# Kernel tuning notes

Measured on AMD Instinct MI355X. Metric: run time of the kernel, lower is better.

## Reference

```python
import jax, jax.numpy as jnp
import numpy as np

EPS = 1e-5


def setup_inputs() -> dict:
    key = jax.random.key(0)
    k1, k2 = jax.random.split(key)
    M, K, N = 8192, 4096, 11008  # tokens, in_features, out_features
    x = jax.random.normal(k1, (M, K), dtype=jnp.float32)
    w = jax.random.normal(k2, (N, K), dtype=jnp.float32)  # Linear weight [out, in]
    return {"x": x, "w": w}


def reference(x, w):
    # --- weight quantization (done once in __init__ in the torch module) ---
    # per-output-channel abs-max scale, clamped
    w_scales = jnp.maximum(jnp.max(jnp.abs(w), axis=1, keepdims=True), EPS) / 127.0  # [N,1]
    w_int8 = jnp.round(w / w_scales).astype(jnp.int8)  # [N,K]

    # --- dynamic per-token activation quantization ---
    x_scales = jnp.maximum(jnp.max(jnp.abs(x), axis=-1, keepdims=True), EPS) / 127.0  # [M,1]
    x_int8 = jnp.round(x / x_scales).astype(jnp.int8)  # [M,K]

    # --- int8 GEMM with int32 accumulation (torch._int_mm) ---
    out_int32 = jnp.matmul(x_int8.astype(jnp.int32), w_int8.T.astype(jnp.int32))  # [M,N]

    # --- dequantize: per-token scale x per-channel scale ---
    return out_int32.astype(x.dtype) * (x_scales * w_scales.reshape(1, -1))
```

## Files before the change

kernel.cpp:

```cpp
#include <hip/hip_runtime.h>
#include <hip/hip_bf16.h>


#define QEPS 1e-5f

using int4v = __attribute__((ext_vector_type(4))) int;

typedef __attribute__((address_space(3))) signed char lds_i8_t;
typedef __attribute__((address_space(1))) const signed char glb_i8_t;

__global__ __launch_bounds__(256) void quant_rows_k(const float* __restrict__ in,
                                                    signed char* __restrict__ out8,
                                                    float* __restrict__ scales) {
    const int K = 4096;
    const int row = blockIdx.x;
    const int t = threadIdx.x;
    const float4* in4 = (const float4*)(in + (size_t)row * K);
    float4 v[4];
    float amax = 0.f;
#pragma unroll
    for (int j = 0; j < 4; ++j) {
        v[j] = in4[t + 256 * j];
        amax = fmaxf(amax, fmaxf(fmaxf(fabsf(v[j].x), fabsf(v[j].y)),
                                 fmaxf(fabsf(v[j].z), fabsf(v[j].w))));
    }
#pragma unroll
    for (int off = 32; off > 0; off >>= 1)
        amax = fmaxf(amax, __shfl_xor(amax, off));
    __shared__ float wmax[4];
    if ((t & 63) == 0) wmax[t >> 6] = amax;
    __syncthreads();
    amax = fmaxf(fmaxf(wmax[0], wmax[1]), fmaxf(wmax[2], wmax[3]));
    const float scale = fmaxf(amax, QEPS) / 127.0f;
    if (t == 0) scales[row] = scale;
    char4* o4 = (char4*)(out8 + (size_t)row * K);
#pragma unroll
    for (int j = 0; j < 4; ++j) {
        char4 q;
        q.x = (signed char)(int)rintf(v[j].x / scale);
        q.y = (signed char)(int)rintf(v[j].y / scale);
        q.z = (signed char)(int)rintf(v[j].z / scale);
        q.w = (signed char)(int)rintf(v[j].w / scale);
        o4[t + 256 * j] = q;
    }
}

__global__ __launch_bounds__(512, 2) void gemm_i8_256(const signed char* __restrict__ A,
                                                      const signed char* __restrict__ B,
                                                      const float* __restrict__ xs,
                                                      const float* __restrict__ wsc,
                                                      float* __restrict__ C) {
    constexpr int K = 4096;
    constexpr int N = 11008;
    constexpr int BK = 128;
    constexpr int NT = K / BK;
    constexpr int TILE = 256 * 128;

    __shared__ __align__(16) signed char lds[4 * TILE];
    signed char* const la0 = lds;
    signed char* const la1 = lds + TILE;
    signed char* const lb0 = lds + 2 * TILE;
    signed char* const lb1 = lds + 3 * TILE;

    const int t = threadIdx.x;
    const int lane = t & 63;
    const int wid = t >> 6;
    const int wr = wid >> 2;
    const int wc = wid & 3;

    const int wg = (blockIdx.x & 7) * ((int)gridDim.x >> 3) + ((int)blockIdx.x >> 3);
    const int by = wg / 43;
    const int bx = wg - by * 43;
    const int brow = by * 256;
    const int bcol = bx * 256;

    const int srow = t >> 3;
    const int scol = ((t & 7) * 16) ^ ((srow & 7) << 4);
    const signed char* aptr = A + (size_t)(brow + srow) * K + scol;
    const signed char* bptr = B + (size_t)(bcol + srow) * K + scol;

    const int arow0 = wr * 128 + (lane & 15);
    const int bcol0 = wc * 64 + (lane & 15);
    const int kgrp = (lane >> 4) * 16;
    const int sw = (lane & 7) << 4;

    int4v acc[8][4];
#pragma unroll
    for (int m = 0; m < 8; ++m)
#pragma unroll
        for (int n = 0; n < 4; ++n) acc[m][n] = (int4v){0, 0, 0, 0};

#define STAGE(LA, LB, KT)                                                                  \
    do {                                                                                   \
        _Pragma("unroll") for (int j = 0; j < 4; ++j)                                      \
            __builtin_amdgcn_global_load_lds(                                              \
                (glb_i8_t*)(aptr + (size_t)(j * 64) * K + (size_t)(KT)*BK),                \
                (lds_i8_t*)((LA) + (j * 512 + t) * 16), 16, 0, 0);                         \
        _Pragma("unroll") for (int j = 0; j < 4; ++j)                                      \
            __builtin_amdgcn_global_load_lds(                                              \
                (glb_i8_t*)(bptr + (size_t)(j * 64) * K + (size_t)(KT)*BK),                \
                (lds_i8_t*)((LB) + (j * 512 + t) * 16), 16, 0, 0);                         \
    } while (0)

    auto compute_tile = [&](const signed char* LA, const signed char* LB) {
#pragma unroll
        for (int ks = 0; ks < 2; ++ks) {
            int4v bf[4];
#pragma unroll
            for (int n = 0; n < 4; ++n)
                bf[n] = *(const int4v*)(LB + (bcol0 + n * 16) * 128 + ((ks * 64 + kgrp) ^ sw));
#pragma unroll
            for (int mh = 0; mh < 2; ++mh) {
                int4v af[4];
#pragma unroll
                for (int mi = 0; mi < 4; ++mi)
                    af[mi] = *(const int4v*)(LA + (arow0 + (mh * 4 + mi) * 16) * 128 +
                                             ((ks * 64 + kgrp) ^ sw));
                __builtin_amdgcn_s_setprio(1);
#pragma unroll
                for (int mi = 0; mi < 4; ++mi)
#pragma unroll
                    for (int n = 0; n < 4; ++n)
                        acc[mh * 4 + mi][n] = __builtin_amdgcn_mfma_i32_16x16x64_i8(
                            af[mi], bf[n], acc[mh * 4 + mi][n], 0, 0, 0);
                __builtin_amdgcn_s_setprio(0);
            }
        }
    };

    STAGE(la0, lb0, 0);
    STAGE(la1, lb1, 1);
    asm volatile("s_waitcnt vmcnt(8)" ::: "memory");
    __builtin_amdgcn_s_barrier();

#pragma unroll 1
    for (int kt = 0; kt < NT; kt += 2) {
        compute_tile(la0, lb0);
        __builtin_amdgcn_s_barrier();
        STAGE(la0, lb0, (kt + 2) & (NT - 1));
        asm volatile("s_waitcnt vmcnt(8)" ::: "memory");
        __builtin_amdgcn_s_barrier();
        compute_tile(la1, lb1);
        __builtin_amdgcn_s_barrier();
        STAGE(la1, lb1, (kt + 3) & (NT - 1));
        asm volatile("s_waitcnt vmcnt(8)" ::: "memory");
        __builtin_amdgcn_s_barrier();
    }
#undef STAGE

    const int rgrp = (lane >> 4) * 4;
    float wsv[4];
#pragma unroll
    for (int n = 0; n < 4; ++n) wsv[n] = wsc[bcol + wc * 64 + n * 16 + (lane & 15)];
#pragma unroll
    for (int m = 0; m < 8; ++m) {
#pragma unroll
        for (int r = 0; r < 4; ++r) {
            const int row = brow + wr * 128 + m * 16 + rgrp + r;
            const float xsv = xs[row];
            const size_t base = (size_t)row * N + bcol + wc * 64 + (lane & 15);
#pragma unroll
            for (int n = 0; n < 4; ++n)
                C[base + n * 16] = (float)acc[m][n][r] * (xsv * wsv[n]);
        }
    }
}

extern "C" void kernel_launch(void* const* d_in, const int* in_sizes, int n_in,
                              void* d_out, int out_size, void* d_ws, size_t ws_size,
                              hipStream_t stream) {
    const float* x = (const float*)d_in[0];
    const float* w = (const float*)d_in[1];
    float* out = (float*)d_out;

    const int K = 4096;
    const int M = in_sizes[0] / K;
    const int N = in_sizes[1] / K;

    signed char* x8 = (signed char*)d_ws;
    signed char* w8 = x8 + (size_t)M * K;
    float* xscales = (float*)(w8 + (size_t)N * K);
    float* wscales = xscales + M;

    quant_rows_k<<<M, 256, 0, stream>>>(x, x8, xscales);
    quant_rows_k<<<N, 256, 0, stream>>>(w, w8, wscales);
    const int nwg = (M / 256) * (N / 256);
    gemm_i8_256<<<nwg, 512, 0, stream>>>(x8, w8, xscales, wscales, out);
}
```

Measured before the change: 480.5 us.

## Interleave global-to-LDS prefetch with MFMA in four phases per K-tile

Restructures the int8 GEMM main loop into four phases per 128-wide K tile. Each phase loads fragments from LDS, issues part of the next tile's global_load_lds, then runs 16 MFMAs, so memory traffic is spread across compute instead of issued in bulk between tiles. The LDS layout changes to two 64-byte K halves per buffer without XOR swizzling, which may bring back LDS bank conflicts on fragment reads. It also adds more barriers per tile.

```diff
diff --git a/kernel.cpp b/kernel.cpp
--- a/kernel.cpp
+++ b/kernel.cpp
@@ -45,22 +45,18 @@
     }
 }
 
-__global__ __launch_bounds__(512, 2) void gemm_i8_256(const signed char* __restrict__ A,
+__global__ __launch_bounds__(512, 2) void gemm_i8_8ph(const signed char* __restrict__ A,
                                                       const signed char* __restrict__ B,
                                                       const float* __restrict__ xs,
                                                       const float* __restrict__ wsc,
                                                       float* __restrict__ C) {
     constexpr int K = 4096;
     constexpr int N = 11008;
-    constexpr int BK = 128;
-    constexpr int NT = K / BK;
-    constexpr int TILE = 256 * 128;
+    constexpr int NT = 32;
+    constexpr int HALF = 256 * 64;
 
-    __shared__ __align__(16) signed char lds[4 * TILE];
-    signed char* const la0 = lds;
-    signed char* const la1 = lds + TILE;
-    signed char* const lb0 = lds + 2 * TILE;
-    signed char* const lb1 = lds + 3 * TILE;
+    __shared__ __align__(16) signed char lsA[2][2 * HALF];
+    __shared__ __align__(16) signed char lsB[2][2 * HALF];
 
     const int t = threadIdx.x;
     const int lane = t & 63;
@@ -74,15 +70,16 @@
     const int brow = by * 256;
     const int bcol = bx * 256;
 
-    const int srow = t >> 3;
-    const int scol = ((t & 7) * 16) ^ ((srow & 7) << 4);
-    const signed char* aptr = A + (size_t)(brow + srow) * K + scol;
-    const signed char* bptr = B + (size_t)(bcol + srow) * K + scol;
+    const int srow = t >> 2;
+    const int sc = (t & 3) * 16;
+    const signed char* aSrc0 = A + (size_t)(brow + srow) * K + sc;
+    const signed char* aSrc1 = aSrc0 + (size_t)128 * K;
+    const signed char* bSrc0 = B + (size_t)(bcol + srow) * K + sc;
+    const signed char* bSrc1 = bSrc0 + (size_t)128 * K;
 
     const int arow0 = wr * 128 + (lane & 15);
     const int bcol0 = wc * 64 + (lane & 15);
     const int kgrp = (lane >> 4) * 16;
-    const int sw = (lane & 7) << 4;
 
     int4v acc[8][4];
 #pragma unroll
@@ -90,63 +87,66 @@
 #pragma unroll
         for (int n = 0; n < 4; ++n) acc[m][n] = (int4v){0, 0, 0, 0};
 
-#define STAGE(LA, LB, KT)                                                                  \
-    do {                                                                                   \
-        _Pragma("unroll") for (int j = 0; j < 4; ++j)                                      \
-            __builtin_amdgcn_global_load_lds(                                              \
-                (glb_i8_t*)(aptr + (size_t)(j * 64) * K + (size_t)(KT)*BK),                \
-                (lds_i8_t*)((LA) + (j * 512 + t) * 16), 16, 0, 0);                         \
-        _Pragma("unroll") for (int j = 0; j < 4; ++j)                                      \
-            __builtin_amdgcn_global_load_lds(                                              \
-                (glb_i8_t*)(bptr + (size_t)(j * 64) * K + (size_t)(KT)*BK),                \
-                (lds_i8_t*)((LB) + (j * 512 + t) * 16), 16, 0, 0);                         \
+#define STAGE2(DST, S0, S1, OFFK)                                                         \
+    do {                                                                                  \
+        __builtin_amdgcn_global_load_lds((glb_i8_t*)((S0) + (OFFK)),                      \
+                                         (lds_i8_t*)((DST) + t * 16), 16, 0, 0);          \
+        __builtin_amdgcn_global_load_lds((glb_i8_t*)((S1) + (OFFK)),                      \
+                                         (lds_i8_t*)((DST) + 8192 + t * 16), 16, 0, 0);   \
     } while (0)
 
-    auto compute_tile = [&](const signed char* LA, const signed char* LB) {
-#pragma unroll
-        for (int ks = 0; ks < 2; ++ks) {
-            int4v bf[4];
-#pragma unroll
-            for (int n = 0; n < 4; ++n)
-                bf[n] = *(const int4v*)(LB + (bcol0 + n * 16) * 128 + ((ks * 64 + kgrp) ^ sw));
-#pragma unroll
-            for (int mh = 0; mh < 2; ++mh) {
-                int4v af[4];
-#pragma unroll
-                for (int mi = 0; mi < 4; ++mi)
-                    af[mi] = *(const int4v*)(LA + (arow0 + (mh * 4 + mi) * 16) * 128 +
-                                             ((ks * 64 + kgrp) ^ sw));
-                __builtin_amdgcn_s_setprio(1);
-#pragma unroll
-                for (int mi = 0; mi < 4; ++mi)
-#pragma unroll
-                    for (int n = 0; n < 4; ++n)
-                        acc[mh * 4 + mi][n] = __builtin_amdgcn_mfma_i32_16x16x64_i8(
-                            af[mi], bf[n], acc[mh * 4 + mi][n], 0, 0, 0);
-                __builtin_amdgcn_s_setprio(0);
-            }
-        }
-    };
+    {
+        signed char* SA = &lsA[0][0];
+        signed char* SB = &lsB[0][0];
+        STAGE2(SA, aSrc0, aSrc1, 0);
+        STAGE2(SB, bSrc0, bSrc1, 0);
+        STAGE2(SA + HALF, aSrc0, aSrc1, 64);
+        STAGE2(SB + HALF, bSrc0, bSrc1, 64);
+        asm volatile("s_waitcnt vmcnt(4)" ::: "memory");
+        __builtin_amdgcn_s_barrier();
+    }
 
-    STAGE(la0, lb0, 0);
-    STAGE(la1, lb1, 1);
-    asm volatile("s_waitcnt vmcnt(8)" ::: "memory");
-    __builtin_amdgcn_s_barrier();
+    int4v bf[4];
+
+#define PHASE(KS, MH, SDST, S0, S1, SOFFK, DOVM)                                          \
+    do {                                                                                  \
+        const signed char* BAks = BA + (KS)*HALF;                                         \
+        const signed char* BBks = BB + (KS)*HALF;                                         \
+        if ((MH) == 0) {                                                                  \
+            _Pragma("unroll") for (int n = 0; n < 4; ++n)                                 \
+                bf[n] = *(const int4v*)(BBks + (bcol0 + n * 16) * 64 + kgrp);             \
+        }                                                                                 \
+        int4v af[4];                                                                      \
+        _Pragma("unroll") for (int mi = 0; mi < 4; ++mi)                                  \
+            af[mi] = *(const int4v*)(BAks + (arow0 + (MH)*64 + mi * 16) * 64 + kgrp);     \
+        STAGE2((SDST), (S0), (S1), (SOFFK));                                              \
+        if (DOVM) asm volatile("s_waitcnt vmcnt(4)" ::: "memory");                        \
+        __builtin_amdgcn_s_barrier();                                                     \
+        __builtin_amdgcn_s_setprio(1);                                                    \
+        _Pragma("unroll") for (int mi = 0; mi < 4; ++mi)                                  \
+            _Pragma("unroll") for (int n = 0; n < 4; ++n)                                 \
+                acc[(MH)*4 + mi][n] = __builtin_amdgcn_mfma_i32_16x16x64_i8(              \
+                    af[mi], bf[n], acc[(MH)*4 + mi][n], 0, 0, 0);                         \
+        __builtin_amdgcn_s_setprio(0);                                                    \
+        __builtin_amdgcn_s_barrier();                                                     \
+    } while (0)
 
 #pragma unroll 1
-    for (int kt = 0; kt < NT; kt += 2) {
-        compute_tile(la0, lb0);
-        __builtin_amdgcn_s_barrier();
-        STAGE(la0, lb0, (kt + 2) & (NT - 1));
-        asm volatile("s_waitcnt vmcnt(8)" ::: "memory");
-        __builtin_amdgcn_s_barrier();
-        compute_tile(la1, lb1);
-        __builtin_amdgcn_s_barrier();
-        STAGE(la1, lb1, (kt + 3) & (NT - 1));
-        asm volatile("s_waitcnt vmcnt(8)" ::: "memory");
-        __builtin_amdgcn_s_barrier();
+    for (int u = 0; u < NT; ++u) {
+        const int buf = u & 1;
+        const signed char* BA = &lsA[buf][0];
+        const signed char* BB = &lsB[buf][0];
+        signed char* SA = &lsA[buf ^ 1][0];
+        signed char* SB = &lsB[buf ^ 1][0];
+        const size_t off0 = (size_t)((u + 1) & (NT - 1)) * 128;
+
+        PHASE(0, 0, SA, aSrc0, aSrc1, off0, 0);
+        PHASE(0, 1, SB, bSrc0, bSrc1, off0, 1);
+        PHASE(1, 0, SA + HALF, aSrc0, aSrc1, off0 + 64, 0);
+        PHASE(1, 1, SB + HALF, bSrc0, bSrc1, off0 + 64, 1);
     }
-#undef STAGE
+#undef PHASE
+#undef STAGE2
 
     const int rgrp = (lane >> 4) * 4;
     float wsv[4];
@@ -185,5 +185,5 @@
     quant_rows_k<<<M, 256, 0, stream>>>(x, x8, xscales);
     quant_rows_k<<<N, 256, 0, stream>>>(w, w8, wscales);
     const int nwg = (M / 256) * (N / 256);
-    gemm_i8_256<<<nwg, 512, 0, stream>>>(x8, w8, xscales, wscales, out);
+    gemm_i8_8ph<<<nwg, 512, 0, stream>>>(x8, w8, xscales, wscales, out);
 }
```

Result: slower. 588.9 us (+22.6%).

## Switch GEMM to four-stage BK=64 LDS ring with paired compute per barrier

Applied to the files above, without the earlier changes.

Halves the K tile to 64 and uses a four-buffer LDS ring in place of double buffering with BK=128. Each loop iteration computes two tiles, then refills both buffers with one barrier pair, so barriers per K step are halved. The LDS swizzle is reworked for 64-byte rows. Total LDS stays at 128KB, but prefetch depth grows while each load batch gets smaller, with possible changes in bank conflicts and latency hiding.

```diff
diff --git a/kernel.cpp b/kernel.cpp
--- a/kernel.cpp
+++ b/kernel.cpp
@@ -45,22 +45,19 @@
     }
 }
 
-__global__ __launch_bounds__(512, 2) void gemm_i8_256(const signed char* __restrict__ A,
-                                                      const signed char* __restrict__ B,
-                                                      const float* __restrict__ xs,
-                                                      const float* __restrict__ wsc,
-                                                      float* __restrict__ C) {
+__global__ __launch_bounds__(512, 2) void gemm_i8_q4(const signed char* __restrict__ A,
+                                                     const signed char* __restrict__ B,
+                                                     const float* __restrict__ xs,
+                                                     const float* __restrict__ wsc,
+                                                     float* __restrict__ C) {
     constexpr int K = 4096;
     constexpr int N = 11008;
-    constexpr int BK = 128;
+    constexpr int BK = 64;
     constexpr int NT = K / BK;
-    constexpr int TILE = 256 * 128;
+    constexpr int TILE = 256 * BK;
 
-    __shared__ __align__(16) signed char lds[4 * TILE];
-    signed char* const la0 = lds;
-    signed char* const la1 = lds + TILE;
-    signed char* const lb0 = lds + 2 * TILE;
-    signed char* const lb1 = lds + 3 * TILE;
+    __shared__ __align__(16) signed char lsA[4][TILE];
+    __shared__ __align__(16) signed char lsB[4][TILE];
 
     const int t = threadIdx.x;
     const int lane = t & 63;
@@ -74,15 +71,14 @@
     const int brow = by * 256;
     const int bcol = bx * 256;
 
-    const int srow = t >> 3;
-    const int scol = ((t & 7) * 16) ^ ((srow & 7) << 4);
-    const signed char* aptr = A + (size_t)(brow + srow) * K + scol;
-    const signed char* bptr = B + (size_t)(bcol + srow) * K + scol;
+    const int srow = t >> 2;
+    const int scol = ((t & 3) * 16) ^ ((((t >> 3)) & 3) << 4);
+    const signed char* aSrc = A + (size_t)(brow + srow) * K + scol;
+    const signed char* bSrc = B + (size_t)(bcol + srow) * K + scol;
 
     const int arow0 = wr * 128 + (lane & 15);
     const int bcol0 = wc * 64 + (lane & 15);
-    const int kgrp = (lane >> 4) * 16;
-    const int sw = (lane & 7) << 4;
+    const int colf = ((lane >> 4) * 16) ^ ((((lane & 15) >> 1) & 3) << 4);
 
     int4v acc[8][4];
 #pragma unroll
@@ -90,59 +86,52 @@
 #pragma unroll
         for (int n = 0; n < 4; ++n) acc[m][n] = (int4v){0, 0, 0, 0};
 
-#define STAGE(LA, LB, KT)                                                                  \
+#define STAGE(BUF, KT)                                                                     \
     do {                                                                                   \
-        _Pragma("unroll") for (int j = 0; j < 4; ++j)                                      \
-            __builtin_amdgcn_global_load_lds(                                              \
-                (glb_i8_t*)(aptr + (size_t)(j * 64) * K + (size_t)(KT)*BK),                \
-                (lds_i8_t*)((LA) + (j * 512 + t) * 16), 16, 0, 0);                         \
-        _Pragma("unroll") for (int j = 0; j < 4; ++j)                                      \
-            __builtin_amdgcn_global_load_lds(                                              \
-                (glb_i8_t*)(bptr + (size_t)(j * 64) * K + (size_t)(KT)*BK),                \
-                (lds_i8_t*)((LB) + (j * 512 + t) * 16), 16, 0, 0);                         \
+        const size_t ko = (size_t)(KT)*BK;                                                 \
+        __builtin_amdgcn_global_load_lds((glb_i8_t*)(aSrc + ko),                           \
+                                         (lds_i8_t*)(&lsA[BUF][0] + t * 16), 16, 0, 0);    \
+        __builtin_amdgcn_global_load_lds((glb_i8_t*)(aSrc + (size_t)128 * K + ko),         \
+                                         (lds_i8_t*)(&lsA[BUF][8192] + t * 16), 16, 0, 0); \
+        __builtin_amdgcn_global_load_lds((glb_i8_t*)(bSrc + ko),                           \
+                                         (lds_i8_t*)(&lsB[BUF][0] + t * 16), 16, 0, 0);    \
+        __builtin_amdgcn_global_load_lds((glb_i8_t*)(bSrc + (size_t)128 * K + ko),         \
+                                         (lds_i8_t*)(&lsB[BUF][8192] + t * 16), 16, 0, 0); \
     } while (0)
 
     auto compute_tile = [&](const signed char* LA, const signed char* LB) {
+        int4v bf[4];
 #pragma unroll
-        for (int ks = 0; ks < 2; ++ks) {
-            int4v bf[4];
+        for (int n = 0; n < 4; ++n)
+            bf[n] = *(const int4v*)(LB + (bcol0 + n * 16) * 64 + colf);
+        int4v af[8];
+#pragma unroll
+        for (int mi = 0; mi < 8; ++mi)
+            af[mi] = *(const int4v*)(LA + (arow0 + mi * 16) * 64 + colf);
+        __builtin_amdgcn_s_setprio(1);
+#pragma unroll
+        for (int mi = 0; mi < 8; ++mi)
 #pragma unroll
             for (int n = 0; n < 4; ++n)
-                bf[n] = *(const int4v*)(LB + (bcol0 + n * 16) * 128 + ((ks * 64 + kgrp) ^ sw));
-#pragma unroll
-            for (int mh = 0; mh < 2; ++mh) {
-                int4v af[4];
-#pragma unroll
-                for (int mi = 0; mi < 4; ++mi)
-                    af[mi] = *(const int4v*)(LA + (arow0 + (mh * 4 + mi) * 16) * 128 +
-                                             ((ks * 64 + kgrp) ^ sw));
-                __builtin_amdgcn_s_setprio(1);
-#pragma unroll
-                for (int mi = 0; mi < 4; ++mi)
-#pragma unroll
-                    for (int n = 0; n < 4; ++n)
-                        acc[mh * 4 + mi][n] = __builtin_amdgcn_mfma_i32_16x16x64_i8(
-                            af[mi], bf[n], acc[mh * 4 + mi][n], 0, 0, 0);
-                __builtin_amdgcn_s_setprio(0);
-            }
-        }
+                acc[mi][n] = __builtin_amdgcn_mfma_i32_16x16x64_i8(af[mi], bf[n],
+                                                                   acc[mi][n], 0, 0, 0);
+        __builtin_amdgcn_s_setprio(0);
     };
 
-    STAGE(la0, lb0, 0);
-    STAGE(la1, lb1, 1);
+    STAGE(0, 0);
+    STAGE(1, 1);
+    STAGE(2, 2);
+    STAGE(3, 3);
     asm volatile("s_waitcnt vmcnt(8)" ::: "memory");
     __builtin_amdgcn_s_barrier();
 
 #pragma unroll 1
-    for (int kt = 0; kt < NT; kt += 2) {
-        compute_tile(la0, lb0);
+    for (int u = 0; u < NT; u += 2) {
+        compute_tile(&lsA[u & 3][0], &lsB[u & 3][0]);
+        compute_tile(&lsA[(u + 1) & 3][0], &lsB[(u + 1) & 3][0]);
         __builtin_amdgcn_s_barrier();
-        STAGE(la0, lb0, (kt + 2) & (NT - 1));
-        asm volatile("s_waitcnt vmcnt(8)" ::: "memory");
-        __builtin_amdgcn_s_barrier();
-        compute_tile(la1, lb1);
-        __builtin_amdgcn_s_barrier();
-        STAGE(la1, lb1, (kt + 3) & (NT - 1));
+        STAGE(u & 3, (u + 4) & (NT - 1));
+        STAGE((u + 1) & 3, (u + 5) & (NT - 1));
         asm volatile("s_waitcnt vmcnt(8)" ::: "memory");
         __builtin_amdgcn_s_barrier();
     }
@@ -185,5 +174,5 @@
     quant_rows_k<<<M, 256, 0, stream>>>(x, x8, xscales);
     quant_rows_k<<<N, 256, 0, stream>>>(w, w8, wscales);
     const int nwg = (M / 256) * (N / 256);
-    gemm_i8_256<<<nwg, 512, 0, stream>>>(x8, w8, xscales, wscales, out);
+    gemm_i8_q4<<<nwg, 512, 0, stream>>>(x8, w8, xscales, wscales, out);
 }
```

Result: slower. 572.5 us (+19.1%).

## Interleave global-to-LDS prefetch with MFMA phases in an eight-phase pipeline

Applied to the files above, without the earlier changes.

Restructures the int8 GEMM main loop so each K-tile is split into four compute phases, each preceded by a partial global_load_lds issue for the next tile and a barrier plus lgkmcnt wait. The prefetch traffic is spread across the MFMA work instead of issued in bulk between whole tiles, aiming to keep the matrix cores fed and hide memory latency. It adds more barriers per tile and finer vmcnt bookkeeping, which adds synchronisation overhead and a risk of ordering mistakes.

```diff
diff --git a/kernel.cpp b/kernel.cpp
--- a/kernel.cpp
+++ b/kernel.cpp
@@ -45,22 +45,19 @@
     }
 }
 
-__global__ __launch_bounds__(512, 2) void gemm_i8_256(const signed char* __restrict__ A,
-                                                      const signed char* __restrict__ B,
-                                                      const float* __restrict__ xs,
-                                                      const float* __restrict__ wsc,
-                                                      float* __restrict__ C) {
+__global__ __launch_bounds__(512, 2) void gemm_i8_8p(const signed char* __restrict__ A,
+                                                     const signed char* __restrict__ B,
+                                                     const float* __restrict__ xs,
+                                                     const float* __restrict__ wsc,
+                                                     float* __restrict__ C) {
     constexpr int K = 4096;
     constexpr int N = 11008;
     constexpr int BK = 128;
-    constexpr int NT = K / BK;
+    constexpr int NT = 32;
     constexpr int TILE = 256 * 128;
 
-    __shared__ __align__(16) signed char lds[4 * TILE];
-    signed char* const la0 = lds;
-    signed char* const la1 = lds + TILE;
-    signed char* const lb0 = lds + 2 * TILE;
-    signed char* const lb1 = lds + 3 * TILE;
+    __shared__ __align__(16) signed char lsA[2][TILE];
+    __shared__ __align__(16) signed char lsB[2][TILE];
 
     const int t = threadIdx.x;
     const int lane = t & 63;
@@ -90,63 +87,84 @@
 #pragma unroll
         for (int n = 0; n < 4; ++n) acc[m][n] = (int4v){0, 0, 0, 0};
 
-#define STAGE(LA, LB, KT)                                                                  \
-    do {                                                                                   \
-        _Pragma("unroll") for (int j = 0; j < 4; ++j)                                      \
-            __builtin_amdgcn_global_load_lds(                                              \
-                (glb_i8_t*)(aptr + (size_t)(j * 64) * K + (size_t)(KT)*BK),                \
-                (lds_i8_t*)((LA) + (j * 512 + t) * 16), 16, 0, 0);                         \
-        _Pragma("unroll") for (int j = 0; j < 4; ++j)                                      \
-            __builtin_amdgcn_global_load_lds(                                              \
-                (glb_i8_t*)(bptr + (size_t)(j * 64) * K + (size_t)(KT)*BK),                \
-                (lds_i8_t*)((LB) + (j * 512 + t) * 16), 16, 0, 0);                         \
-    } while (0)
-
-    auto compute_tile = [&](const signed char* LA, const signed char* LB) {
-#pragma unroll
-        for (int ks = 0; ks < 2; ++ks) {
-            int4v bf[4];
-#pragma unroll
-            for (int n = 0; n < 4; ++n)
-                bf[n] = *(const int4v*)(LB + (bcol0 + n * 16) * 128 + ((ks * 64 + kgrp) ^ sw));
-#pragma unroll
-            for (int mh = 0; mh < 2; ++mh) {
-                int4v af[4];
-#pragma unroll
-                for (int mi = 0; mi < 4; ++mi)
-                    af[mi] = *(const int4v*)(LA + (arow0 + (mh * 4 + mi) * 16) * 128 +
-                                             ((ks * 64 + kgrp) ^ sw));
-                __builtin_amdgcn_s_setprio(1);
-#pragma unroll
-                for (int mi = 0; mi < 4; ++mi)
-#pragma unroll
-                    for (int n = 0; n < 4; ++n)
-                        acc[mh * 4 + mi][n] = __builtin_amdgcn_mfma_i32_16x16x64_i8(
-                            af[mi], bf[n], acc[mh * 4 + mi][n], 0, 0, 0);
-                __builtin_amdgcn_s_setprio(0);
-            }
-        }
-    };
-
-    STAGE(la0, lb0, 0);
-    STAGE(la1, lb1, 1);
-    asm volatile("s_waitcnt vmcnt(8)" ::: "memory");
+#define LDA_(J, KOFF, SB)                                                                  \
+    __builtin_amdgcn_global_load_lds((glb_i8_t*)(aptr + (size_t)((J)*64) * K + (KOFF)),    \
+                                     (lds_i8_t*)(&lsA[SB][0] + ((J)*512 + t) * 16), 16, 0, 0)
+#define LDB_(J, KOFF, SB)                                                                  \
+    __builtin_amdgcn_global_load_lds((glb_i8_t*)(bptr + (size_t)((J)*64) * K + (KOFF)),    \
+                                     (lds_i8_t*)(&lsB[SB][0] + ((J)*512 + t) * 16), 16, 0, 0)
+
+    LDB_(0, 0, 0); LDB_(1, 0, 0); LDB_(2, 0, 0); LDB_(3, 0, 0);
+    LDA_(0, 0, 0); LDA_(2, 0, 0); LDA_(1, 0, 0); LDA_(3, 0, 0);
+    asm volatile("s_waitcnt vmcnt(2)" ::: "memory");
     __builtin_amdgcn_s_barrier();
 
+    int4v bf0[4], bf1[4];
+
+#define MFMA16(MH, BF)                                                                     \
+    __builtin_amdgcn_s_setprio(1);                                                         \
+    _Pragma("unroll") for (int mi = 0; mi < 4; ++mi)                                       \
+        _Pragma("unroll") for (int n = 0; n < 4; ++n)                                      \
+            acc[(MH)*4 + mi][n] = __builtin_amdgcn_mfma_i32_16x16x64_i8(                   \
+                af[mi], BF[n], acc[(MH)*4 + mi][n], 0, 0, 0);                              \
+    __builtin_amdgcn_s_setprio(0);                                                         \
+    __builtin_amdgcn_s_barrier();
+
+#define BAR_LGKM()                                                                         \
+    __builtin_amdgcn_s_barrier();                                                          \
+    asm volatile("s_waitcnt lgkmcnt(0)" ::: "memory");                                     \
+    __builtin_amdgcn_sched_barrier(0);
+
 #pragma unroll 1
-    for (int kt = 0; kt < NT; kt += 2) {
-        compute_tile(la0, lb0);
-        __builtin_amdgcn_s_barrier();
-        STAGE(la0, lb0, (kt + 2) & (NT - 1));
-        asm volatile("s_waitcnt vmcnt(8)" ::: "memory");
-        __builtin_amdgcn_s_barrier();
-        compute_tile(la1, lb1);
-        __builtin_amdgcn_s_barrier();
-        STAGE(la1, lb1, (kt + 3) & (NT - 1));
-        asm volatile("s_waitcnt vmcnt(8)" ::: "memory");
-        __builtin_amdgcn_s_barrier();
-    }
-#undef STAGE
+    for (int u = 0; u < NT; ++u) {
+        const int cb = u & 1, sb = cb ^ 1;
+        const signed char* cA = &lsA[cb][0];
+        const signed char* cB = &lsB[cb][0];
+        const size_t koff = (size_t)((u + 1) & (NT - 1)) * BK;
+        int4v af[4];
+
+#pragma unroll
+        for (int n = 0; n < 4; ++n)
+            bf0[n] = *(const int4v*)(cB + (bcol0 + n * 16) * 128 + (kgrp ^ sw));
+#pragma unroll
+        for (int mi = 0; mi < 4; ++mi)
+            af[mi] = *(const int4v*)(cA + (arow0 + mi * 16) * 128 + (kgrp ^ sw));
+        LDB_(0, koff, sb); LDB_(1, koff, sb);
+        BAR_LGKM();
+        MFMA16(0, bf0);
+
+#pragma unroll
+        for (int n = 0; n < 4; ++n)
+            bf1[n] = *(const int4v*)(cB + (bcol0 + n * 16) * 128 + ((64 + kgrp) ^ sw));
+#pragma unroll
+        for (int mi = 0; mi < 4; ++mi)
+            af[mi] = *(const int4v*)(cA + (arow0 + mi * 16) * 128 + ((64 + kgrp) ^ sw));
+        LDB_(2, koff, sb); LDB_(3, koff, sb);
+        asm volatile("s_waitcnt vmcnt(4)" ::: "memory");
+        BAR_LGKM();
+        MFMA16(0, bf1);
+
+#pragma unroll
+        for (int mi = 0; mi < 4; ++mi)
+            af[mi] = *(const int4v*)(cA + (arow0 + 64 + mi * 16) * 128 + (kgrp ^ sw));
+        LDA_(0, koff, sb); LDA_(2, koff, sb);
+        BAR_LGKM();
+        MFMA16(1, bf0);
+
+#pragma unroll
+        for (int mi = 0; mi < 4; ++mi)
+            af[mi] = *(const int4v*)(cA + (arow0 + 64 + mi * 16) * 128 + ((64 + kgrp) ^ sw));
+        LDA_(1, koff, sb); LDA_(3, koff, sb);
+        asm volatile("s_waitcnt vmcnt(2)" ::: "memory");
+        BAR_LGKM();
+        MFMA16(1, bf1);
+    }
+#undef MFMA16
+#undef BAR_LGKM
+#undef LDA_
+#undef LDB_
+
+    asm volatile("s_waitcnt vmcnt(0)" ::: "memory");
 
     const int rgrp = (lane >> 4) * 4;
     float wsv[4];
@@ -185,5 +203,5 @@
     quant_rows_k<<<M, 256, 0, stream>>>(x, x8, xscales);
     quant_rows_k<<<N, 256, 0, stream>>>(w, w8, wscales);
     const int nwg = (M / 256) * (N / 256);
-    gemm_i8_256<<<nwg, 512, 0, stream>>>(x8, w8, xscales, wscales, out);
+    gemm_i8_8p<<<nwg, 512, 0, stream>>>(x8, w8, xscales, wscales, out);
 }
```

Result: slower. 498.3 us (+3.7%).
